# Performance work log

Measured on AMD Instinct MI355X. Metric: run time of the kernel, lower is better.

The kernel has to match this reference:

```python
import jax, jax.numpy as jnp
import numpy as np

T, L = 8192, 16          # sentence length, chars per word (fixed-length regularization)
EW, EC = 256, 64         # word / char embedding dims
H, H2 = 512, 128         # final / char LSTM hidden dims
V, C, TAGS = 100000, 128, 64


def setup_inputs() -> dict:
    key = jax.random.key(0)
    ks = jax.random.split(key, 12)
    p = lambda k, shape: jax.random.normal(k, shape, dtype=jnp.float32) * 0.02
    return {
        'sentence': jax.random.randint(ks[0], (T,), 0, V, dtype=jnp.int32),
        'seq_chars': jax.random.randint(ks[1], (T, L), 0, C, dtype=jnp.int32),
        'emb_word': p(ks[2], (V, EW)),
        'emb_char': p(ks[3], (C, EC)),
        'Wih_c': p(ks[4], (4 * H2, EC)),   # char LSTM input weights (i,f,g,o)
        'Whh_c': p(ks[5], (4 * H2, H2)),
        'b_c':   p(ks[6], (4 * H2,)),      # b_ih + b_hh fused
        'Wih_f': p(ks[7], (4 * H, EW + H2)),
        'Whh_f': p(ks[8], (4 * H, H)),
        'b_f':   p(ks[9], (4 * H,)),
        'W_tag': p(ks[10], (TAGS, H)),
        'b_tag': p(ks[11], (TAGS,)),
    }


def _lstm_step(W_ih, W_hh, b, carry, x_t):
    # PyTorch LSTM cell, gate order i, f, g, o
    h, c = carry
    gates = x_t @ W_ih.T + h @ W_hh.T + b
    i, f, g, o = jnp.split(gates, 4, axis=-1)
    c = jax.nn.sigmoid(f) * c + jax.nn.sigmoid(i) * jnp.tanh(g)
    h = jax.nn.sigmoid(o) * jnp.tanh(c)
    return (h, c), h


def reference(sentence, seq_chars, emb_word, emb_char,
              Wih_c, Whh_c, b_c, Wih_f, Whh_f, b_f, W_tag, b_tag):
    Tn = sentence.shape[0]
    h2 = Whh_c.shape[1]
    hd = Whh_f.shape[1]

    ew = emb_word[sentence]            # (T, EW)
    ec = emb_char[seq_chars]           # (T, L, EC)

    # char LSTM: all T words batched together, scan over char positions
    xc = jnp.swapaxes(ec, 0, 1)        # (L, T, EC)
    z2 = jnp.zeros((Tn, h2), dtype=ew.dtype)
    step_c = lambda carry, x: _lstm_step(Wih_c, Whh_c, b_c, carry, x)
    (h_char, _), _ = jax.lax.scan(step_c, (z2, z2), xc)   # final hidden per word (T, H2)

    # final word-level LSTM over the sentence (batch = 1)
    x_fin = jnp.concatenate([ew, h_char], axis=-1)        # (T, EW + H2)
    zh = jnp.zeros((hd,), dtype=ew.dtype)
    step_f = lambda carry, x: _lstm_step(Wih_f, Whh_f, b_f, carry, x)
    _, h_seq = jax.lax.scan(step_f, (zh, zh), x_fin)      # (T, H)

    logits = h_seq @ W_tag.T + b_tag                      # (T, TAGS)
    return jax.nn.log_softmax(logits, axis=-1)
```

## Files before the change

### kernel.cpp

```cpp
#include <hip/hip_runtime.h>

#define T_LEN 8192
#define L_CH  16
#define EW    256
#define EC    64
#define HID   512
#define H2    128
#define TAGS  64

#define NBLK_REC 16
#define A_WORDS  16

__global__ void k_init(unsigned long long* hbuf) {
    int t = threadIdx.x;
    for (int i = t; i < 2 * HID; i += blockDim.x)
        hbuf[i] = (i < HID) ? (1ULL << 32) : 0ULL;
}

__global__ __launch_bounds__(256) void k_char(const int* __restrict__ seq_chars,
                                              const float* __restrict__ emb_char,
                                              const float* __restrict__ Wih,
                                              const float* __restrict__ Whh,
                                              const float* __restrict__ bc,
                                              float* __restrict__ h_char) {
    __shared__ float xs[A_WORDS][76];
    __shared__ float hs[A_WORDS][132];
    __shared__ float cs[A_WORDS][128];
    __shared__ float gs[A_WORDS][512];

    const int tid = threadIdx.x;
    const int w0  = blockIdx.x * A_WORDS;

    for (int i = tid; i < A_WORDS * 132; i += 256) hs[i / 132][i % 132] = 0.f;
    for (int i = tid; i < A_WORDS * 128; i += 256) cs[i >> 7][i & 127] = 0.f;

    const int rowg = tid >> 2;
    const int wg   = tid & 3;
    const int r0   = rowg * 8;
    const int wb   = wg * 4;

    float bias_r[8];
#pragma unroll
    for (int r = 0; r < 8; ++r) bias_r[r] = bc[r0 + r];

    for (int l = 0; l < L_CH; ++l) {
        __syncthreads();
        {
            int w = tid >> 4, p = tid & 15;
            int ci = seq_chars[(w0 + w) * L_CH + l];
            float4 v = ((const float4*)emb_char)[ci * 16 + p];
            *(float4*)&xs[w][p * 4] = v;
        }
        __syncthreads();

        float acc[8][4];
#pragma unroll
        for (int r = 0; r < 8; ++r)
#pragma unroll
            for (int w = 0; w < 4; ++w) acc[r][w] = bias_r[r];

#pragma unroll 4
        for (int k4 = 0; k4 < 16; ++k4) {
            float4 wv[8];
#pragma unroll
            for (int r = 0; r < 8; ++r) wv[r] = ((const float4*)Wih)[(r0 + r) * 16 + k4];
#pragma unroll
            for (int w = 0; w < 4; ++w) {
                const float4 xv = *(const float4*)&xs[wb + w][k4 * 4];
#pragma unroll
                for (int r = 0; r < 8; ++r)
                    acc[r][w] += wv[r].x * xv.x + wv[r].y * xv.y + wv[r].z * xv.z + wv[r].w * xv.w;
            }
        }
#pragma unroll 2
        for (int k4 = 0; k4 < 32; ++k4) {
            float4 wv[8];
#pragma unroll
            for (int r = 0; r < 8; ++r) wv[r] = ((const float4*)Whh)[(r0 + r) * 32 + k4];
#pragma unroll
            for (int w = 0; w < 4; ++w) {
                const float4 hv = *(const float4*)&hs[wb + w][k4 * 4];
#pragma unroll
                for (int r = 0; r < 8; ++r)
                    acc[r][w] += wv[r].x * hv.x + wv[r].y * hv.y + wv[r].z * hv.z + wv[r].w * hv.w;
            }
        }
#pragma unroll
        for (int r = 0; r < 8; ++r)
#pragma unroll
            for (int w = 0; w < 4; ++w) gs[wb + w][r0 + r] = acc[r][w];
        __syncthreads();

        {
            int w = tid >> 4;
            int j0 = (tid & 15) * 8;
#pragma unroll
            for (int u = 0; u < 8; ++u) {
                int j = j0 + u;
                float gi = gs[w][j], gf = gs[w][128 + j], gg = gs[w][256 + j], go = gs[w][384 + j];
                float si = 1.f / (1.f + __expf(-gi));
                float sf = 1.f / (1.f + __expf(-gf));
                float so = 1.f / (1.f + __expf(-go));
                float tg = 1.f - 2.f / (__expf(2.f * gg) + 1.f);
                float c  = sf * cs[w][j] + si * tg;
                cs[w][j] = c;
                hs[w][j] = so * (1.f - 2.f / (__expf(2.f * c) + 1.f));
            }
        }
    }
    __syncthreads();
    for (int i = tid; i < A_WORDS * (H2 / 4); i += 256) {
        int w = i >> 5, p = i & 31;
        ((float4*)h_char)[(w0 + w) * 32 + p] = *(float4*)&hs[w][p * 4];
    }
}

__global__ void k_gather(const int* __restrict__ sentence, const float* __restrict__ emb_word,
                         const float* __restrict__ h_char, float* __restrict__ x_fin) {
    int i = blockIdx.x * blockDim.x + threadIdx.x;
    const int total = T_LEN * 96;
    for (; i < total; i += gridDim.x * blockDim.x) {
        int word = i / 96, s = i % 96;
        float4 v;
        if (s < 64) v = ((const float4*)emb_word)[(size_t)sentence[word] * 64 + s];
        else        v = ((const float4*)h_char)[word * 32 + (s - 64)];
        ((float4*)x_fin)[i] = v;
    }
}

__global__ __launch_bounds__(256) void k_pregemm(const float* __restrict__ A,
                                                 const float* __restrict__ B,
                                                 const float* __restrict__ bias,
                                                 float* __restrict__ Cm) {
    __shared__ float As[16][128];
    __shared__ float Bs[16][128];
    const int tid = threadIdx.x;
    const int M0 = blockIdx.x * 128;
    const int N0 = blockIdx.y * 128;
    const int tx = tid & 15, ty = tid >> 4;

    float acc[8][8];
#pragma unroll
    for (int i = 0; i < 8; ++i)
#pragma unroll
        for (int j = 0; j < 8; ++j) acc[i][j] = 0.f;

    float bcol[8];
#pragma unroll
    for (int j = 0; j < 8; ++j) bcol[j] = bias[N0 + tx * 8 + j];

    const int r  = tid >> 1;
    const int kq = (tid & 1) * 8;

    for (int k0 = 0; k0 < 384; k0 += 16) {
        __syncthreads();
        {
            const float4* A4 = (const float4*)A;
            const float4* B4 = (const float4*)B;
            float4 a0 = A4[(M0 + r) * 96 + (k0 + kq) / 4];
            float4 a1 = A4[(M0 + r) * 96 + (k0 + kq) / 4 + 1];
            float4 b0 = B4[(N0 + r) * 96 + (k0 + kq) / 4];
            float4 b1 = B4[(N0 + r) * 96 + (k0 + kq) / 4 + 1];
            As[kq + 0][r] = a0.x; As[kq + 1][r] = a0.y; As[kq + 2][r] = a0.z; As[kq + 3][r] = a0.w;
            As[kq + 4][r] = a1.x; As[kq + 5][r] = a1.y; As[kq + 6][r] = a1.z; As[kq + 7][r] = a1.w;
            Bs[kq + 0][r] = b0.x; Bs[kq + 1][r] = b0.y; Bs[kq + 2][r] = b0.z; Bs[kq + 3][r] = b0.w;
            Bs[kq + 4][r] = b1.x; Bs[kq + 5][r] = b1.y; Bs[kq + 6][r] = b1.z; Bs[kq + 7][r] = b1.w;
        }
        __syncthreads();
#pragma unroll
        for (int k = 0; k < 16; ++k) {
            float a[8], b[8];
            *(float4*)&a[0] = *(const float4*)&As[k][ty * 8];
            *(float4*)&a[4] = *(const float4*)&As[k][ty * 8 + 4];
            *(float4*)&b[0] = *(const float4*)&Bs[k][tx * 8];
            *(float4*)&b[4] = *(const float4*)&Bs[k][tx * 8 + 4];
#pragma unroll
            for (int i = 0; i < 8; ++i)
#pragma unroll
                for (int j = 0; j < 8; ++j) acc[i][j] += a[i] * b[j];
        }
    }
    const int n_base = N0 + tx * 8;
#pragma unroll
    for (int i = 0; i < 8; ++i) {
        int m = M0 + ty * 8 + i;
        float4 o0 = make_float4(acc[i][0] + bcol[0], acc[i][1] + bcol[1], acc[i][2] + bcol[2], acc[i][3] + bcol[3]);
        float4 o1 = make_float4(acc[i][4] + bcol[4], acc[i][5] + bcol[5], acc[i][6] + bcol[6], acc[i][7] + bcol[7]);
        float4* C4 = (float4*)(Cm + (size_t)m * 2048 + n_base);
        C4[0] = o0; C4[1] = o1;
    }
}

__global__ __launch_bounds__(512, 2) void k_rec(const float* __restrict__ pre,
                                                const float* __restrict__ Whh,
                                                unsigned long long* hbuf,
                                                float* __restrict__ h_seq) {
    const int tid = threadIdx.x;
    const int b   = blockIdx.x;
    const int ksl = tid & 15;
    const int rq  = tid >> 4;
    const int typ = rq >> 3;
    const int row_lo = (4 * rq) & 31;
    const int grow0  = typ * HID + b * 32 + row_lo;

    float w[4][32];
#pragma unroll
    for (int j = 0; j < 4; ++j) {
        const float4* Wr = (const float4*)(Whh + (size_t)(grow0 + j) * HID + ksl * 32);
#pragma unroll
        for (int i = 0; i < 8; ++i) {
            float4 v = Wr[i];
            w[j][4 * i] = v.x; w[j][4 * i + 1] = v.y; w[j][4 * i + 2] = v.z; w[j][4 * i + 3] = v.w;
        }
    }

    __shared__ __align__(16) float h_lds[16 * 36];
    __shared__ __align__(16) float act[128];
    const int st_pos = (tid >> 5) * 36 + (tid & 31);

    float c = 0.f;
    const int jglob = b * 32 + (tid & 31);
    const bool pl = (ksl == 0);

    float4 pre_cur = make_float4(0.f, 0.f, 0.f, 0.f);
    if (pl) pre_cur = *(const float4*)&pre[grow0];

    for (int step = 0; step < T_LEN; ++step) {
        float4 pre_nxt = make_float4(0.f, 0.f, 0.f, 0.f);
        if (pl && step + 1 < T_LEN)
            pre_nxt = *(const float4*)&pre[(size_t)(step + 1) * 2048 + grow0];

        {
            unsigned long long* wp = &hbuf[(step & 1) * HID + tid];
            const unsigned want = (unsigned)(step + 1);
            unsigned long long vv = __hip_atomic_load(wp, __ATOMIC_RELAXED, __HIP_MEMORY_SCOPE_AGENT);
            while ((unsigned)(vv >> 32) != want) {
                __builtin_amdgcn_s_sleep(1);
                vv = __hip_atomic_load(wp, __ATOMIC_RELAXED, __HIP_MEMORY_SCOPE_AGENT);
            }
            h_lds[st_pos] = __uint_as_float((unsigned)vv);
        }
        __syncthreads();

        float acc0 = 0.f, acc1 = 0.f, acc2 = 0.f, acc3 = 0.f;
        {
            const float* hb = &h_lds[ksl * 36];
#pragma unroll
            for (int i = 0; i < 8; ++i) {
                float4 hv = *(const float4*)(hb + 4 * i);
                acc0 += w[0][4 * i] * hv.x + w[0][4 * i + 1] * hv.y + w[0][4 * i + 2] * hv.z + w[0][4 * i + 3] * hv.w;
                acc1 += w[1][4 * i] * hv.x + w[1][4 * i + 1] * hv.y + w[1][4 * i + 2] * hv.z + w[1][4 * i + 3] * hv.w;
                acc2 += w[2][4 * i] * hv.x + w[2][4 * i + 1] * hv.y + w[2][4 * i + 2] * hv.z + w[2][4 * i + 3] * hv.w;
                acc3 += w[3][4 * i] * hv.x + w[3][4 * i + 1] * hv.y + w[3][4 * i + 2] * hv.z + w[3][4 * i + 3] * hv.w;
            }
        }
#pragma unroll
        for (int o = 1; o <= 8; o <<= 1) {
            acc0 += __shfl_xor(acc0, o, 64);
            acc1 += __shfl_xor(acc1, o, 64);
            acc2 += __shfl_xor(acc2, o, 64);
            acc3 += __shfl_xor(acc3, o, 64);
        }

        if (pl) {
            float g0 = acc0 + pre_cur.x;
            float g1 = acc1 + pre_cur.y;
            float g2 = acc2 + pre_cur.z;
            float g3 = acc3 + pre_cur.w;
            float4 a;
            if (typ == 2) {
                a.x = 1.f - 2.f / (__expf(2.f * g0) + 1.f);
                a.y = 1.f - 2.f / (__expf(2.f * g1) + 1.f);
                a.z = 1.f - 2.f / (__expf(2.f * g2) + 1.f);
                a.w = 1.f - 2.f / (__expf(2.f * g3) + 1.f);
            } else {
                a.x = 1.f / (1.f + __expf(-g0));
                a.y = 1.f / (1.f + __expf(-g1));
                a.z = 1.f / (1.f + __expf(-g2));
                a.w = 1.f / (1.f + __expf(-g3));
            }
            *(float4*)&act[4 * rq] = a;
        }
        __syncthreads();

        if (tid < 32) {
            float si = act[tid], sf = act[32 + tid], tg = act[64 + tid], so = act[96 + tid];
            c = sf * c + si * tg;
            float h = so * (1.f - 2.f / (__expf(2.f * c) + 1.f));
            h_seq[(size_t)step * HID + jglob] = h;
            unsigned long long pack = (((unsigned long long)(unsigned)(step + 2)) << 32)
                                      | (unsigned long long)__float_as_uint(h);
            __hip_atomic_store(&hbuf[((step + 1) & 1) * HID + jglob], pack,
                               __ATOMIC_RELAXED, __HIP_MEMORY_SCOPE_AGENT);
        }
        pre_cur = pre_nxt;
    }
}

__global__ __launch_bounds__(256) void k_tag(const float* __restrict__ h_seq,
                                             const float* __restrict__ Wt,
                                             const float* __restrict__ bt,
                                             float* __restrict__ out) {
    const int tid  = threadIdx.x;
    const int lane = tid & 63;
    const int word = blockIdx.x * 4 + (tid >> 6);
    const float4* W4 = (const float4*)Wt;
    const float4* h4 = (const float4*)(h_seq + (size_t)word * HID);
    float acc = bt[lane];
#pragma unroll 8
    for (int k = 0; k < 128; ++k) {
        float4 a = W4[lane * 128 + k];
        float4 h = h4[k];
        acc += a.x * h.x + a.y * h.y + a.z * h.z + a.w * h.w;
    }
    float m = acc;
#pragma unroll
    for (int o = 32; o >= 1; o >>= 1) m = fmaxf(m, __shfl_xor(m, o, 64));
    float e = __expf(acc - m);
    float s = e;
#pragma unroll
    for (int o = 32; o >= 1; o >>= 1) s += __shfl_xor(s, o, 64);
    out[(size_t)word * TAGS + lane] = acc - m - __logf(s);
}

extern "C" void kernel_launch(void* const* d_in, const int* in_sizes, int n_in,
                              void* d_out, int out_size, void* d_ws, size_t ws_size,
                              hipStream_t stream) {
    const int*   sentence  = (const int*)d_in[0];
    const int*   seq_chars = (const int*)d_in[1];
    const float* emb_word  = (const float*)d_in[2];
    const float* emb_char  = (const float*)d_in[3];
    const float* Wih_c     = (const float*)d_in[4];
    const float* Whh_c     = (const float*)d_in[5];
    const float* b_c       = (const float*)d_in[6];
    const float* Wih_f     = (const float*)d_in[7];
    const float* Whh_f     = (const float*)d_in[8];
    const float* b_f       = (const float*)d_in[9];
    const float* W_tag     = (const float*)d_in[10];
    const float* b_tag     = (const float*)d_in[11];
    float* out = (float*)d_out;

    float* ws     = (float*)d_ws;
    float* h_char = ws;
    float* x_fin  = h_char + (size_t)T_LEN * H2;
    float* pre    = x_fin  + (size_t)T_LEN * 384;
    float* h_seq  = pre    + (size_t)T_LEN * 2048;
    unsigned long long* hbuf = (unsigned long long*)(h_seq + (size_t)T_LEN * HID);

    hipLaunchKernelGGL(k_init,   dim3(1),               dim3(256), 0, stream, hbuf);
    hipLaunchKernelGGL(k_char,   dim3(T_LEN / A_WORDS), dim3(256), 0, stream,
                       seq_chars, emb_char, Wih_c, Whh_c, b_c, h_char);
    hipLaunchKernelGGL(k_gather, dim3(1024),            dim3(256), 0, stream,
                       sentence, emb_word, h_char, x_fin);
    hipLaunchKernelGGL(k_pregemm, dim3(64, 16),         dim3(256), 0, stream,
                       x_fin, Wih_f, b_f, pre);
    hipLaunchKernelGGL(k_rec,    dim3(NBLK_REC),        dim3(512), 0, stream,
                       pre, Whh_f, hbuf, h_seq);
    hipLaunchKernelGGL(k_tag,    dim3(T_LEN / 4),       dim3(256), 0, stream,
                       h_seq, W_tag, b_tag, out);
}
```

Baseline: 18.03 ms.

## Double recurrent-kernel threads so each thread computes two gate rows instead of four

The sequential word-level LSTM kernel now runs 1024 threads per block, with each thread holding two rows of the recurrent weight slice in registers instead of four. This halves the per-thread dot-product and shuffle-reduction work on the serial critical path per timestep. The cost is more waves contending in the block-wide barriers. The h_seq store is also moved after the atomic publish of h, so other blocks can see the new state sooner.

```diff
diff --git a/kernel.cpp b/kernel.cpp
--- a/kernel.cpp
+++ b/kernel.cpp
@@ -191,28 +191,33 @@
     }
 }
 
-__global__ __launch_bounds__(512, 2) void k_rec(const float* __restrict__ pre,
-                                                const float* __restrict__ Whh,
-                                                unsigned long long* hbuf,
-                                                float* __restrict__ h_seq) {
+__global__ __launch_bounds__(1024, 4) void k_rec(const float* __restrict__ pre,
+                                                 const float* __restrict__ Whh,
+                                                 unsigned long long* hbuf,
+                                                 float* __restrict__ h_seq) {
     const int tid = threadIdx.x;
     const int b   = blockIdx.x;
     const int ksl = tid & 15;
-    const int rq  = tid >> 4;
-    const int typ = rq >> 3;
-    const int row_lo = (4 * rq) & 31;
-    const int grow0  = typ * HID + b * 32 + row_lo;
-
-    float w[4][32];
-#pragma unroll
-    for (int j = 0; j < 4; ++j) {
-        const float4* Wr = (const float4*)(Whh + (size_t)(grow0 + j) * HID + ksl * 32);
+    const int rp  = tid >> 4;
+    const int typ = rp >> 4;
+    const int jj0 = (2 * rp) & 31;
+    const int grow0 = typ * HID + b * 32 + jj0;
+
+    float w0[32], w1[32];
+    {
+        const float4* Wr0 = (const float4*)(Whh + (size_t)grow0 * HID + ksl * 32);
+        const float4* Wr1 = (const float4*)(Whh + (size_t)(grow0 + 1) * HID + ksl * 32);
 #pragma unroll
         for (int i = 0; i < 8; ++i) {
-            float4 v = Wr[i];
-            w[j][4 * i] = v.x; w[j][4 * i + 1] = v.y; w[j][4 * i + 2] = v.z; w[j][4 * i + 3] = v.w;
-        }
-    }
+            float4 v0 = Wr0[i];
+            w0[4 * i] = v0.x; w0[4 * i + 1] = v0.y; w0[4 * i + 2] = v0.z; w0[4 * i + 3] = v0.w;
+            float4 v1 = Wr1[i];
+            w1[4 * i] = v1.x; w1[4 * i + 1] = v1.y; w1[4 * i + 2] = v1.z; w1[4 * i + 3] = v1.w;
+        }
+    }
+#pragma unroll
+    for (int i = 0; i < 32; ++i)
+        asm volatile("" : "+v"(w0[i]), "+v"(w1[i]));
 
     __shared__ __align__(16) float h_lds[16 * 36];
     __shared__ __align__(16) float act[128];
@@ -222,15 +227,15 @@
     const int jglob = b * 32 + (tid & 31);
     const bool pl = (ksl == 0);
 
-    float4 pre_cur = make_float4(0.f, 0.f, 0.f, 0.f);
-    if (pl) pre_cur = *(const float4*)&pre[grow0];
+    float2 pre_cur = make_float2(0.f, 0.f);
+    if (pl) pre_cur = *(const float2*)&pre[grow0];
 
     for (int step = 0; step < T_LEN; ++step) {
-        float4 pre_nxt = make_float4(0.f, 0.f, 0.f, 0.f);
+        float2 pre_nxt = make_float2(0.f, 0.f);
         if (pl && step + 1 < T_LEN)
-            pre_nxt = *(const float4*)&pre[(size_t)(step + 1) * 2048 + grow0];
-
-        {
+            pre_nxt = *(const float2*)&pre[(size_t)(step + 1) * 2048 + grow0];
+
+        if (tid < 512) {
             unsigned long long* wp = &hbuf[(step & 1) * HID + tid];
             const unsigned want = (unsigned)(step + 1);
             unsigned long long vv = __hip_atomic_load(wp, __ATOMIC_RELAXED, __HIP_MEMORY_SCOPE_AGENT);
@@ -242,44 +247,34 @@
         }
         __syncthreads();
 
-        float acc0 = 0.f, acc1 = 0.f, acc2 = 0.f, acc3 = 0.f;
+        float acc0 = 0.f, acc1 = 0.f;
         {
             const float* hb = &h_lds[ksl * 36];
 #pragma unroll
             for (int i = 0; i < 8; ++i) {
                 float4 hv = *(const float4*)(hb + 4 * i);
-                acc0 += w[0][4 * i] * hv.x + w[0][4 * i + 1] * hv.y + w[0][4 * i + 2] * hv.z + w[0][4 * i + 3] * hv.w;
-                acc1 += w[1][4 * i] * hv.x + w[1][4 * i + 1] * hv.y + w[1][4 * i + 2] * hv.z + w[1][4 * i + 3] * hv.w;
-                acc2 += w[2][4 * i] * hv.x + w[2][4 * i + 1] * hv.y + w[2][4 * i + 2] * hv.z + w[2][4 * i + 3] * hv.w;
-                acc3 += w[3][4 * i] * hv.x + w[3][4 * i + 1] * hv.y + w[3][4 * i + 2] * hv.z + w[3][4 * i + 3] * hv.w;
+                acc0 += w0[4 * i] * hv.x + w0[4 * i + 1] * hv.y + w0[4 * i + 2] * hv.z + w0[4 * i + 3] * hv.w;
+                acc1 += w1[4 * i] * hv.x + w1[4 * i + 1] * hv.y + w1[4 * i + 2] * hv.z + w1[4 * i + 3] * hv.w;
             }
         }
 #pragma unroll
         for (int o = 1; o <= 8; o <<= 1) {
             acc0 += __shfl_xor(acc0, o, 64);
             acc1 += __shfl_xor(acc1, o, 64);
-            acc2 += __shfl_xor(acc2, o, 64);
-            acc3 += __shfl_xor(acc3, o, 64);
         }
 
         if (pl) {
             float g0 = acc0 + pre_cur.x;
             float g1 = acc1 + pre_cur.y;
-            float g2 = acc2 + pre_cur.z;
-            float g3 = acc3 + pre_cur.w;
-            float4 a;
+            float2 a;
             if (typ == 2) {
                 a.x = 1.f - 2.f / (__expf(2.f * g0) + 1.f);
                 a.y = 1.f - 2.f / (__expf(2.f * g1) + 1.f);
-                a.z = 1.f - 2.f / (__expf(2.f * g2) + 1.f);
-                a.w = 1.f - 2.f / (__expf(2.f * g3) + 1.f);
             } else {
                 a.x = 1.f / (1.f + __expf(-g0));
                 a.y = 1.f / (1.f + __expf(-g1));
-                a.z = 1.f / (1.f + __expf(-g2));
-                a.w = 1.f / (1.f + __expf(-g3));
-            }
-            *(float4*)&act[4 * rq] = a;
+            }
+            *(float2*)&act[2 * rp] = a;
         }
         __syncthreads();
 
@@ -287,11 +282,11 @@
             float si = act[tid], sf = act[32 + tid], tg = act[64 + tid], so = act[96 + tid];
             c = sf * c + si * tg;
             float h = so * (1.f - 2.f / (__expf(2.f * c) + 1.f));
-            h_seq[(size_t)step * HID + jglob] = h;
             unsigned long long pack = (((unsigned long long)(unsigned)(step + 2)) << 32)
                                       | (unsigned long long)__float_as_uint(h);
             __hip_atomic_store(&hbuf[((step + 1) & 1) * HID + jglob], pack,
                                __ATOMIC_RELAXED, __HIP_MEMORY_SCOPE_AGENT);
+            h_seq[(size_t)step * HID + jglob] = h;
         }
         pre_cur = pre_nxt;
     }
@@ -354,7 +349,7 @@
                        sentence, emb_word, h_char, x_fin);
     hipLaunchKernelGGL(k_pregemm, dim3(64, 16),         dim3(256), 0, stream,
                        x_fin, Wih_f, b_f, pre);
-    hipLaunchKernelGGL(k_rec,    dim3(NBLK_REC),        dim3(512), 0, stream,
+    hipLaunchKernelGGL(k_rec,    dim3(NBLK_REC),        dim3(1024), 0, stream,
                        pre, Whh_f, hbuf, h_seq);
     hipLaunchKernelGGL(k_tag,    dim3(T_LEN / 4),       dim3(256), 0, stream,
                        h_seq, W_tag, b_tag, out);
```

Result: faster. 17.41 ms (-3.4%).
